# Performance work log

Measured on AMD Instinct MI355X. Metric: run time of the kernel, lower is better.

## Reference

```python
import jax, jax.numpy as jnp
import numpy as np

H = 6      # n_attention_heads
BLK = 64


def adder1x1(x2d, w):
    """AdderNet 1x1 'convolution': Y[co, n] = -sum_ci |x2d[ci, n] - w[co, ci]|.
    Processed in output-channel blocks to bound the abs-diff intermediate.
    x2d: [Ci, N], w: [Co, Ci] -> [Co, N]
    """
    co, ci = w.shape
    wb = w.reshape(co // BLK, BLK, ci)
    def f(wblk):  # wblk: [BLK, Ci] -> [BLK, N]
        return -jnp.sum(jnp.abs(x2d[None, :, :] - wblk[:, :, None]), axis=1)
    return jax.lax.map(f, wb).reshape(co, -1)


def layernorm_all(y, w, b, eps=1e-5):
    # nn.LayerNorm([E, B, S]) applied to [1, E, B, S]: normalize over ALL of E,B,S
    mu = jnp.mean(y)
    var = jnp.mean((y - mu) ** 2)
    return (y - mu) * jax.lax.rsqrt(var + eps) * w + b


def layernorm_last(y, w, b, eps=1e-5):
    mu = jnp.mean(y, axis=-1, keepdims=True)
    var = jnp.mean((y - mu) ** 2, axis=-1, keepdims=True)
    return (y - mu) * jax.lax.rsqrt(var + eps) * w + b


def setup_inputs() -> dict:
    key = jax.random.key(0)
    ks = jax.random.split(key, 14)
    B, S, E = 8, 197, 384
    inp = {
        "x": jax.random.normal(ks[0], (B, S, E), jnp.float32),
        "wq": jax.random.normal(ks[1], (E, E), jnp.float32) * 0.05,
        "wk": jax.random.normal(ks[2], (E, E), jnp.float32) * 0.05,
        "wv": jax.random.normal(ks[3], (E, E), jnp.float32) * 0.05,
        "qln_w": 1.0 + 0.02 * jax.random.normal(ks[4], (E, B, S), jnp.float32),
        "qln_b": 0.02 * jax.random.normal(ks[5], (E, B, S), jnp.float32),
        "kln_w": 1.0 + 0.02 * jax.random.normal(ks[6], (E, B, S), jnp.float32),
        "kln_b": 0.02 * jax.random.normal(ks[7], (E, B, S), jnp.float32),
        "vln_w": 1.0 + 0.02 * jax.random.normal(ks[8], (E, B, S), jnp.float32),
        "vln_b": 0.02 * jax.random.normal(ks[9], (E, B, S), jnp.float32),
        "oln_w": 1.0 + 0.02 * jax.random.normal(ks[10], (E,), jnp.float32),
        "oln_b": 0.02 * jax.random.normal(ks[11], (E,), jnp.float32),
        "fc_w": jax.random.normal(ks[12], (E, E), jnp.float32) * 0.05,
        "fc_b": 0.02 * jax.random.normal(ks[13], (E,), jnp.float32),
    }
    return inp


def reference(x, wq, wk, wv, qln_w, qln_b, kln_w, kln_b, vln_w, vln_b,
              oln_w, oln_b, fc_w, fc_b):
    B, S, E = x.shape
    D = E // H
    scale = (2.0 * D * (1.0 - 2.0 / np.pi)) ** (-0.5)

    # torch: x.reshape(1, E, B, S) on contiguous [B,S,E] is a flat-buffer reshape
    x2d = x.reshape(E, B * S)  # [Ci, N]

    def proj(w, lw, lb):
        y = adder1x1(x2d, w).reshape(E, B, S)          # adder2d 1x1, bias=False
        y = layernorm_all(y, lw, lb)                    # LN over [E,B,S]
        y = y.reshape(B, S, H, D)                       # flat reshape (as torch)
        y = jnp.swapaxes(y, 1, 2)                       # [B,H,S,D]
        return y.reshape(B * H, S, D)

    q = proj(wq, qln_w, qln_b)
    k = proj(wk, kln_w, kln_b)
    v = proj(wv, vln_w, vln_b)

    att = jnp.einsum('bsd,btd->bst', q, k) * scale      # [B*H, S, S]
    att = jax.nn.softmax(att, axis=-1) + jnp.eye(S, dtype=x.dtype)
    o = jnp.einsum('bst,btd->bsd', att, v)              # [B*H, S, D]

    o = jnp.swapaxes(o.reshape(B, H, S, D), 1, 2).reshape(B, S, E)
    o = layernorm_last(o, oln_w, oln_b)
    return o @ fc_w.T + fc_b
```

## Files before the change

### kernel.cpp

```cpp
#include <hip/hip_runtime.h>
#include <math.h>

#ifndef M_PI
#define M_PI 3.14159265358979323846
#endif

#define B_ 8
#define S_ 197
#define E_ 384
#define H_ 6
#define D_ 64
#define N_ (B_*S_)
#define EN ((size_t)E_*N_)
#define ATT_LD 200
#define NBLK_ADD 150

__global__ __launch_bounds__(256) void k_adder(
    const float* __restrict__ x,
    const float* __restrict__ wq, const float* __restrict__ wk,
    const float* __restrict__ wv,
    float* __restrict__ Y, float* __restrict__ partials)
{
  const int p = blockIdx.z;
  const float* __restrict__ w = (p == 0) ? wq : (p == 1) ? wk : wv;
  const int co0 = blockIdx.x * 64;
  const int n0  = blockIdx.y * 64;

  __shared__ float Xs[16][64];
  __shared__ float Ws[16][64];
  __shared__ float red[8];

  const int tid = threadIdx.x;
  const int tx = tid & 15;
  const int ty = tid >> 4;

  float acc[4][4];
  #pragma unroll
  for (int i = 0; i < 4; ++i)
    #pragma unroll
    for (int j = 0; j < 4; ++j) acc[i][j] = 0.f;

  for (int ci0 = 0; ci0 < E_; ci0 += 16) {
    {
      int r = tid >> 4, c = (tid & 15) * 4;
      int n = n0 + c;
      float4 v = make_float4(0.f, 0.f, 0.f, 0.f);
      if (n + 3 < N_) v = *(const float4*)(x + (size_t)(ci0 + r) * N_ + n);
      *(float4*)(&Xs[r][c]) = v;
    }
    {
      int r = tid >> 2, c = (tid & 3) * 4;
      float4 v = *(const float4*)(w + (size_t)(co0 + r) * E_ + ci0 + c);
      Ws[c + 0][r] = v.x; Ws[c + 1][r] = v.y;
      Ws[c + 2][r] = v.z; Ws[c + 3][r] = v.w;
    }
    __syncthreads();
    #pragma unroll
    for (int cc = 0; cc < 16; ++cc) {
      float4 xv = *(const float4*)(&Xs[cc][tx * 4]);
      float4 wv4 = *(const float4*)(&Ws[cc][ty * 4]);
      float xa[4] = {xv.x, xv.y, xv.z, xv.w};
      float wa[4] = {wv4.x, wv4.y, wv4.z, wv4.w};
      #pragma unroll
      for (int i = 0; i < 4; ++i)
        #pragma unroll
        for (int j = 0; j < 4; ++j)
          acc[i][j] += fabsf(xa[j] - wa[i]);
    }
    __syncthreads();
  }

  float s1 = 0.f, s2 = 0.f;
  const int nb = n0 + tx * 4;
  if (nb + 3 < N_) {
    #pragma unroll
    for (int i = 0; i < 4; ++i) {
      int co = co0 + ty * 4 + i;
      float4 yv;
      yv.x = -acc[i][0]; yv.y = -acc[i][1];
      yv.z = -acc[i][2]; yv.w = -acc[i][3];
      *(float4*)(Y + (size_t)p * EN + (size_t)co * N_ + nb) = yv;
      s1 += yv.x + yv.y + yv.z + yv.w;
      s2 += yv.x * yv.x + yv.y * yv.y + yv.z * yv.z + yv.w * yv.w;
    }
  }
  #pragma unroll
  for (int off = 32; off > 0; off >>= 1) {
    s1 += __shfl_down(s1, off);
    s2 += __shfl_down(s2, off);
  }
  int wid = tid >> 6, lane = tid & 63;
  if (lane == 0) { red[wid * 2] = s1; red[wid * 2 + 1] = s2; }
  __syncthreads();
  if (tid == 0) {
    float t1 = red[0] + red[2] + red[4] + red[6];
    float t2 = red[1] + red[3] + red[5] + red[7];
    int blk = blockIdx.x * gridDim.y + blockIdx.y;
    partials[((size_t)p * NBLK_ADD + blk) * 2 + 0] = t1;
    partials[((size_t)p * NBLK_ADD + blk) * 2 + 1] = t2;
  }
}

__global__ __launch_bounds__(256) void k_stats(
    const float* __restrict__ partials, float* __restrict__ stats)
{
  const int p = blockIdx.x;
  const int tid = threadIdx.x;
  float s1 = 0.f, s2 = 0.f;
  for (int i = tid; i < NBLK_ADD; i += 256) {
    s1 += partials[((size_t)p * NBLK_ADD + i) * 2 + 0];
    s2 += partials[((size_t)p * NBLK_ADD + i) * 2 + 1];
  }
  #pragma unroll
  for (int off = 32; off > 0; off >>= 1) {
    s1 += __shfl_down(s1, off);
    s2 += __shfl_down(s2, off);
  }
  __shared__ float red[8];
  int wid = tid >> 6, lane = tid & 63;
  if (lane == 0) { red[wid * 2] = s1; red[wid * 2 + 1] = s2; }
  __syncthreads();
  if (tid == 0) {
    float S1 = red[0] + red[2] + red[4] + red[6];
    float S2 = red[1] + red[3] + red[5] + red[7];
    float mean = S1 / (float)EN;
    float var = S2 / (float)EN - mean * mean;
    stats[p * 2 + 0] = mean;
    stats[p * 2 + 1] = rsqrtf(var + 1e-5f);
  }
}

__global__ __launch_bounds__(256) void k_lnall(
    const float* __restrict__ Y, const float* __restrict__ stats,
    const float* __restrict__ w0, const float* __restrict__ b0,
    const float* __restrict__ w1, const float* __restrict__ b1,
    const float* __restrict__ w2, const float* __restrict__ b2,
    float* __restrict__ Z)
{
  const int p = blockIdx.y;
  const float* __restrict__ w = (p == 0) ? w0 : (p == 1) ? w1 : w2;
  const float* __restrict__ b = (p == 0) ? b0 : (p == 1) ? b1 : b2;
  const float mean = stats[p * 2 + 0];
  const float rstd = stats[p * 2 + 1];
  size_t i = ((size_t)blockIdx.x * 256 + threadIdx.x) * 4;
  const float* Yp = Y + (size_t)p * EN;
  float* Zp = Z + (size_t)p * EN;
  float4 y = *(const float4*)(Yp + i);
  float4 wv = *(const float4*)(w + i);
  float4 bv = *(const float4*)(b + i);
  float4 z;
  z.x = (y.x - mean) * rstd * wv.x + bv.x;
  z.y = (y.y - mean) * rstd * wv.y + bv.y;
  z.z = (y.z - mean) * rstd * wv.z + bv.z;
  z.w = (y.w - mean) * rstd * wv.w + bv.w;
  *(float4*)(Zp + i) = z;
}

__global__ __launch_bounds__(256) void k_qk(
    const float* __restrict__ zq, const float* __restrict__ zk,
    float* __restrict__ att, float scale)
{
  const int bh = blockIdx.x, b = bh / H_, h = bh % H_;
  const int s0 = blockIdx.y * 64, t0 = blockIdx.z * 64;
  __shared__ float Qs[64][68];
  __shared__ float Ks[64][68];
  const int tid = threadIdx.x;
  {
    int rl = tid >> 4, c4 = (tid & 15) * 4;
    for (int rr = rl; rr < 64; rr += 16) {
      int s = s0 + rr;
      float4 v = make_float4(0.f, 0.f, 0.f, 0.f);
      if (s < S_) v = *(const float4*)(zq + (size_t)(b * S_ + s) * E_ + h * D_ + c4);
      Qs[c4 + 0][rr] = v.x; Qs[c4 + 1][rr] = v.y;
      Qs[c4 + 2][rr] = v.z; Qs[c4 + 3][rr] = v.w;
      int t = t0 + rr;
      float4 u = make_float4(0.f, 0.f, 0.f, 0.f);
      if (t < S_) u = *(const float4*)(zk + (size_t)(b * S_ + t) * E_ + h * D_ + c4);
      Ks[c4 + 0][rr] = u.x; Ks[c4 + 1][rr] = u.y;
      Ks[c4 + 2][rr] = u.z; Ks[c4 + 3][rr] = u.w;
    }
  }
  __syncthreads();
  const int r0 = (tid >> 4) * 4, c0 = (tid & 15) * 4;
  float acc[4][4];
  #pragma unroll
  for (int i = 0; i < 4; ++i)
    #pragma unroll
    for (int j = 0; j < 4; ++j) acc[i][j] = 0.f;
  #pragma unroll 8
  for (int d = 0; d < 64; ++d) {
    float4 q4 = *(const float4*)(&Qs[d][r0]);
    float4 k4 = *(const float4*)(&Ks[d][c0]);
    float qa[4] = {q4.x, q4.y, q4.z, q4.w};
    float ka[4] = {k4.x, k4.y, k4.z, k4.w};
    #pragma unroll
    for (int i = 0; i < 4; ++i)
      #pragma unroll
      for (int j = 0; j < 4; ++j)
        acc[i][j] += qa[i] * ka[j];
  }
  #pragma unroll
  for (int i = 0; i < 4; ++i) {
    int s = s0 + r0 + i;
    if (s < S_) {
      #pragma unroll
      for (int j = 0; j < 4; ++j) {
        int t = t0 + c0 + j;
        if (t < S_)
          att[((size_t)bh * S_ + s) * ATT_LD + t] = acc[i][j] * scale;
      }
    }
  }
}

__global__ __launch_bounds__(256) void k_softmax(float* __restrict__ att)
{
  const int row = blockIdx.x * 4 + (threadIdx.x >> 6);
  const int lane = threadIdx.x & 63;
  const int s = row % S_;
  float* base = att + (size_t)row * ATT_LD;
  float v[4];
  float m = -1e30f;
  #pragma unroll
  for (int j = 0; j < 4; ++j) {
    int t = lane + 64 * j;
    v[j] = (t < S_) ? base[t] : -1e30f;
    m = fmaxf(m, v[j]);
  }
  #pragma unroll
  for (int off = 32; off > 0; off >>= 1) m = fmaxf(m, __shfl_xor(m, off));
  float sum = 0.f;
  #pragma unroll
  for (int j = 0; j < 4; ++j) {
    int t = lane + 64 * j;
    v[j] = (t < S_) ? __expf(v[j] - m) : 0.f;
    sum += v[j];
  }
  #pragma unroll
  for (int off = 32; off > 0; off >>= 1) sum += __shfl_xor(sum, off);
  float inv = 1.f / sum;
  #pragma unroll
  for (int j = 0; j < 4; ++j) {
    int t = lane + 64 * j;
    if (t < S_) base[t] = v[j] * inv + ((t == s) ? 1.f : 0.f);
  }
}

__global__ __launch_bounds__(256) void k_pv(
    const float* __restrict__ att, const float* __restrict__ zv,
    float* __restrict__ obuf)
{
  const int bh = blockIdx.x, b = bh / H_, h = bh % H_;
  const int s0 = blockIdx.y * 64;
  __shared__ float As[64][68];
  __shared__ float Vs[64][68];
  const int tid = threadIdx.x;
  const int r0 = (tid >> 4) * 4, d0 = (tid & 15) * 4;
  float acc[4][4];
  #pragma unroll
  for (int i = 0; i < 4; ++i)
    #pragma unroll
    for (int j = 0; j < 4; ++j) acc[i][j] = 0.f;

  for (int tt = 0; tt < 256; tt += 64) {
    {
      int sl = tid >> 4, t4 = (tid & 15) * 4;
      for (int rr = sl; rr < 64; rr += 16) {
        int s = s0 + rr;
        #pragma unroll
        for (int k = 0; k < 4; ++k) {
          int t = tt + t4 + k;
          float a = 0.f;
          if (s < S_ && t < S_) a = att[((size_t)bh * S_ + s) * ATT_LD + t];
          As[t4 + k][rr] = a;
        }
        int t = tt + rr;
        float4 v = make_float4(0.f, 0.f, 0.f, 0.f);
        if (t < S_) v = *(const float4*)(zv + (size_t)(b * S_ + t) * E_ + h * D_ + t4);
        *(float4*)(&Vs[rr][t4]) = v;
      }
    }
    __syncthreads();
    #pragma unroll 8
    for (int t = 0; t < 64; ++t) {
      float4 a4 = *(const float4*)(&As[t][r0]);
      float4 v4 = *(const float4*)(&Vs[t][d0]);
      float aa[4] = {a4.x, a4.y, a4.z, a4.w};
      float va[4] = {v4.x, v4.y, v4.z, v4.w};
      #pragma unroll
      for (int i = 0; i < 4; ++i)
        #pragma unroll
        for (int j = 0; j < 4; ++j)
          acc[i][j] += aa[i] * va[j];
    }
    __syncthreads();
  }
  #pragma unroll
  for (int i = 0; i < 4; ++i) {
    int s = s0 + r0 + i;
    if (s < S_) {
      float4 o = make_float4(acc[i][0], acc[i][1], acc[i][2], acc[i][3]);
      *(float4*)(obuf + (size_t)(b * S_ + s) * E_ + h * D_ + d0) = o;
    }
  }
}

__global__ __launch_bounds__(256) void k_lnlast(
    const float* __restrict__ obuf,
    const float* __restrict__ lw, const float* __restrict__ lb,
    float* __restrict__ oln)
{
  const int row = blockIdx.x * 4 + (threadIdx.x >> 6);
  const int lane = threadIdx.x & 63;
  const float* base = obuf + (size_t)row * E_;
  float v[6];
  float s1 = 0.f;
  #pragma unroll
  for (int j = 0; j < 6; ++j) { v[j] = base[lane + 64 * j]; s1 += v[j]; }
  #pragma unroll
  for (int off = 32; off > 0; off >>= 1) s1 += __shfl_xor(s1, off);
  float mean = s1 * (1.f / E_);
  float s2 = 0.f;
  #pragma unroll
  for (int j = 0; j < 6; ++j) { float d = v[j] - mean; s2 += d * d; }
  #pragma unroll
  for (int off = 32; off > 0; off >>= 1) s2 += __shfl_xor(s2, off);
  float rstd = rsqrtf(s2 * (1.f / E_) + 1e-5f);
  float* ob = oln + (size_t)row * E_;
  #pragma unroll
  for (int j = 0; j < 6; ++j) {
    int e = lane + 64 * j;
    ob[e] = (v[j] - mean) * rstd * lw[e] + lb[e];
  }
}

__global__ __launch_bounds__(256) void k_fc(
    const float* __restrict__ oln, const float* __restrict__ fcw,
    const float* __restrict__ fcb, float* __restrict__ out)
{
  const int j0 = blockIdx.x * 64, n0 = blockIdx.y * 64;
  __shared__ float Xs[16][64];
  __shared__ float Ws[16][64];
  const int tid = threadIdx.x;
  const int tx = tid & 15, ty = tid >> 4;
  float acc[4][4];
  #pragma unroll
  for (int i = 0; i < 4; ++i)
    #pragma unroll
    for (int j = 0; j < 4; ++j) acc[i][j] = 0.f;

  for (int e0 = 0; e0 < E_; e0 += 16) {
    {
      int nl = tid >> 2, c4 = (tid & 3) * 4;
      int n = n0 + nl;
      float4 v = make_float4(0.f, 0.f, 0.f, 0.f);
      if (n < N_) v = *(const float4*)(oln + (size_t)n * E_ + e0 + c4);
      Xs[c4 + 0][nl] = v.x; Xs[c4 + 1][nl] = v.y;
      Xs[c4 + 2][nl] = v.z; Xs[c4 + 3][nl] = v.w;
      float4 u = *(const float4*)(fcw + (size_t)(j0 + nl) * E_ + e0 + c4);
      Ws[c4 + 0][nl] = u.x; Ws[c4 + 1][nl] = u.y;
      Ws[c4 + 2][nl] = u.z; Ws[c4 + 3][nl] = u.w;
    }
    __syncthreads();
    #pragma unroll
    for (int cc = 0; cc < 16; ++cc) {
      float4 xv = *(const float4*)(&Xs[cc][tx * 4]);
      float4 wv4 = *(const float4*)(&Ws[cc][ty * 4]);
      float xa[4] = {xv.x, xv.y, xv.z, xv.w};
      float wa[4] = {wv4.x, wv4.y, wv4.z, wv4.w};
      #pragma unroll
      for (int i = 0; i < 4; ++i)
        #pragma unroll
        for (int j = 0; j < 4; ++j)
          acc[i][j] += wa[i] * xa[j];
    }
    __syncthreads();
  }
  #pragma unroll
  for (int jj = 0; jj < 4; ++jj) {
    int n = n0 + tx * 4 + jj;
    if (n < N_) {
      int jc = j0 + ty * 4;
      float4 o;
      o.x = acc[0][jj] + fcb[jc + 0];
      o.y = acc[1][jj] + fcb[jc + 1];
      o.z = acc[2][jj] + fcb[jc + 2];
      o.w = acc[3][jj] + fcb[jc + 3];
      *(float4*)(out + (size_t)n * E_ + jc) = o;
    }
  }
}

extern "C" void kernel_launch(void* const* d_in, const int* in_sizes, int n_in,
                              void* d_out, int out_size, void* d_ws, size_t ws_size,
                              hipStream_t stream)
{
  const float* x   = (const float*)d_in[0];
  const float* wq  = (const float*)d_in[1];
  const float* wk  = (const float*)d_in[2];
  const float* wv  = (const float*)d_in[3];
  const float* qw  = (const float*)d_in[4];
  const float* qb  = (const float*)d_in[5];
  const float* kw  = (const float*)d_in[6];
  const float* kb  = (const float*)d_in[7];
  const float* vw  = (const float*)d_in[8];
  const float* vb  = (const float*)d_in[9];
  const float* ow  = (const float*)d_in[10];
  const float* obp = (const float*)d_in[11];
  const float* fcw = (const float*)d_in[12];
  const float* fcb = (const float*)d_in[13];
  float* out = (float*)d_out;
  float* ws  = (float*)d_ws;

  float* Y     = ws;
  float* Z     = Y + 3 * EN;
  float* att   = Z + 3 * EN;
  float* obuf  = att + (size_t)48 * S_ * ATT_LD;
  float* oln   = obuf + EN;
  float* part  = oln + EN;
  float* stats = part + 3 * NBLK_ADD * 2;

  const float scale = (float)pow(2.0 * D_ * (1.0 - 2.0 / M_PI), -0.5);

  k_adder<<<dim3(6, 25, 3), 256, 0, stream>>>(x, wq, wk, wv, Y, part);
  k_stats<<<dim3(3), 256, 0, stream>>>(part, stats);
  k_lnall<<<dim3(591, 3), 256, 0, stream>>>(Y, stats, qw, qb, kw, kb, vw, vb, Z);
  const float* zq = Z;
  const float* zk = Z + EN;
  const float* zv = Z + 2 * EN;
  k_qk<<<dim3(48, 4, 4), 256, 0, stream>>>(zq, zk, att, scale);
  k_softmax<<<dim3(2364), 256, 0, stream>>>(att);
  k_pv<<<dim3(48, 4), 256, 0, stream>>>(att, zv, obuf);
  k_lnlast<<<dim3(394), 256, 0, stream>>>(obuf, ow, obp, oln);
  k_fc<<<dim3(6, 25), 256, 0, stream>>>(oln, fcw, fcb, out);
}
```

Before: 130.7 us.

## Halve adder tile width and prefetch next tile into registers

The adder kernel's N tile shrinks from 64 to 32 columns, which doubles the grid to 900 blocks so more of the GPU's compute units stay busy. Each thread now holds a 4x2 accumulator instead of 4x4. The next X/W slice is loaded from global memory into registers while the current shared-memory tile is being computed, overlapping load latency with compute. The trade-off is less register-level reuse per shared-memory load and more partial-statistic blocks for the stats reduction.

```diff
diff --git a/kernel.cpp b/kernel.cpp
--- a/kernel.cpp
+++ b/kernel.cpp
@@ -13,7 +13,7 @@
 #define N_ (B_*S_)
 #define EN ((size_t)E_*N_)
 #define ATT_LD 200
-#define NBLK_ADD 150
+#define NBLK_ADD 300
 
 __global__ __launch_bounds__(256) void k_adder(
     const float* __restrict__ x,
@@ -24,9 +24,9 @@
   const int p = blockIdx.z;
   const float* __restrict__ w = (p == 0) ? wq : (p == 1) ? wk : wv;
   const int co0 = blockIdx.x * 64;
-  const int n0  = blockIdx.y * 64;
-
-  __shared__ float Xs[16][64];
+  const int n0  = blockIdx.y * 32;
+
+  __shared__ float Xs[16][32];
   __shared__ float Ws[16][64];
   __shared__ float red[8];
 
@@ -34,54 +34,58 @@
   const int tx = tid & 15;
   const int ty = tid >> 4;
 
-  float acc[4][4];
-  #pragma unroll
-  for (int i = 0; i < 4; ++i)
-    #pragma unroll
-    for (int j = 0; j < 4; ++j) acc[i][j] = 0.f;
-
-  for (int ci0 = 0; ci0 < E_; ci0 += 16) {
-    {
-      int r = tid >> 4, c = (tid & 15) * 4;
-      int n = n0 + c;
-      float4 v = make_float4(0.f, 0.f, 0.f, 0.f);
-      if (n + 3 < N_) v = *(const float4*)(x + (size_t)(ci0 + r) * N_ + n);
-      *(float4*)(&Xs[r][c]) = v;
-    }
-    {
-      int r = tid >> 2, c = (tid & 3) * 4;
-      float4 v = *(const float4*)(w + (size_t)(co0 + r) * E_ + ci0 + c);
-      Ws[c + 0][r] = v.x; Ws[c + 1][r] = v.y;
-      Ws[c + 2][r] = v.z; Ws[c + 3][r] = v.w;
-    }
+  const int xr = tid >> 4, xc = (tid & 15) * 2;
+  const int wr = tid >> 2, wc = (tid & 3) * 4;
+
+  const bool xok = (n0 + xc + 1) < N_;
+  const float* xg = x + (size_t)xr * N_ + n0 + xc;
+  const float* wg = w + (size_t)(co0 + wr) * E_ + wc;
+
+  float2 xv = xok ? *(const float2*)xg : make_float2(0.f, 0.f);
+  float4 wv4 = *(const float4*)wg;
+
+  float acc[4][2];
+  #pragma unroll
+  for (int i = 0; i < 4; ++i) { acc[i][0] = 0.f; acc[i][1] = 0.f; }
+
+  #pragma unroll 1
+  for (int t = 0; t < 24; ++t) {
+    if (t > 0) __syncthreads();
+    *(float2*)(&Xs[xr][xc]) = xv;
+    Ws[wc + 0][wr] = wv4.x; Ws[wc + 1][wr] = wv4.y;
+    Ws[wc + 2][wr] = wv4.z; Ws[wc + 3][wr] = wv4.w;
     __syncthreads();
+    if (t < 23) {
+      xg += (size_t)16 * N_;
+      wg += 16;
+      xv = xok ? *(const float2*)xg : make_float2(0.f, 0.f);
+      wv4 = *(const float4*)wg;
+    }
     #pragma unroll
     for (int cc = 0; cc < 16; ++cc) {
-      float4 xv = *(const float4*)(&Xs[cc][tx * 4]);
-      float4 wv4 = *(const float4*)(&Ws[cc][ty * 4]);
-      float xa[4] = {xv.x, xv.y, xv.z, xv.w};
-      float wa[4] = {wv4.x, wv4.y, wv4.z, wv4.w};
+      float2 x2 = *(const float2*)(&Xs[cc][tx * 2]);
+      float4 w4 = *(const float4*)(&Ws[cc][ty * 4]);
+      float xa[2] = {x2.x, x2.y};
+      float wa[4] = {w4.x, w4.y, w4.z, w4.w};
       #pragma unroll
       for (int i = 0; i < 4; ++i)
         #pragma unroll
-        for (int j = 0; j < 4; ++j)
+        for (int j = 0; j < 2; ++j)
           acc[i][j] += fabsf(xa[j] - wa[i]);
     }
-    __syncthreads();
   }
 
   float s1 = 0.f, s2 = 0.f;
-  const int nb = n0 + tx * 4;
-  if (nb + 3 < N_) {
+  const int nb = n0 + tx * 2;
+  if (nb + 1 < N_) {
     #pragma unroll
     for (int i = 0; i < 4; ++i) {
       int co = co0 + ty * 4 + i;
-      float4 yv;
+      float2 yv;
       yv.x = -acc[i][0]; yv.y = -acc[i][1];
-      yv.z = -acc[i][2]; yv.w = -acc[i][3];
-      *(float4*)(Y + (size_t)p * EN + (size_t)co * N_ + nb) = yv;
-      s1 += yv.x + yv.y + yv.z + yv.w;
-      s2 += yv.x * yv.x + yv.y * yv.y + yv.z * yv.z + yv.w * yv.w;
+      *(float2*)(Y + (size_t)p * EN + (size_t)co * N_ + nb) = yv;
+      s1 += yv.x + yv.y;
+      s2 += yv.x * yv.x + yv.y * yv.y;
     }
   }
   #pragma unroll
@@ -422,7 +426,7 @@
 
   const float scale = (float)pow(2.0 * D_ * (1.0 - 2.0 / M_PI), -0.5);
 
-  k_adder<<<dim3(6, 25, 3), 256, 0, stream>>>(x, wq, wk, wv, Y, part);
+  k_adder<<<dim3(6, 50, 3), 256, 0, stream>>>(x, wq, wk, wv, Y, part);
   k_stats<<<dim3(3), 256, 0, stream>>>(part, stats);
   k_lnall<<<dim3(591, 3), 256, 0, stream>>>(Y, stats, qw, qb, kw, kb, vw, vb, Z);
   const float* zq = Z;
```

Measured after the change: 128.4 us. About the same (-1.8%).
